# Kernel tuning notes

Measured on AMD Instinct MI355X. Metric: run time of the kernel, lower is better.

## Reference

```python
import jax, jax.numpy as jnp
import numpy as np

N = 50000
E = 600000
D_IN = 128
HID = 128
OUT = 64


def setup_inputs() -> dict:
    key = jax.random.key(0)
    ks = jax.random.split(key, 12)
    x = jax.random.normal(ks[0], (N, D_IN), dtype=jnp.float32)
    edge_index = jax.random.randint(ks[1], (2, E), 0, N, dtype=jnp.int32)
    def lin(k, fan_in, fan_out):
        lim = 1.0 / np.sqrt(fan_in)
        kw, kb = jax.random.split(k)
        W = jax.random.uniform(kw, (fan_in, fan_out), minval=-lim, maxval=lim, dtype=jnp.float32)
        b = jax.random.uniform(kb, (fan_out,), minval=-lim, maxval=lim, dtype=jnp.float32)
        return W, b
    W1, b1 = lin(ks[2], D_IN, HID)
    W2, b2 = lin(ks[3], HID, HID)
    W3, b3 = lin(ks[4], HID, HID)
    fcW, fcb = lin(ks[5], HID, OUT)
    return {"x": x, "edge_index": edge_index, "W1": W1, "b1": b1,
            "W2": W2, "b2": b2, "W3": W3, "b3": b3, "fcW": fcW, "fcb": fcb}


def _gcn_prep(edge_index):
    # add self loops, compute symmetric normalization deg^-1/2 * deg^-1/2
    loop = jnp.arange(N, dtype=edge_index.dtype)
    src = jnp.concatenate([edge_index[0], loop])
    dst = jnp.concatenate([edge_index[1], loop])
    deg = jax.ops.segment_sum(jnp.ones_like(dst, dtype=jnp.float32), dst, num_segments=N)
    dinv = jnp.where(deg > 0, jax.lax.rsqrt(deg), 0.0)
    norm = dinv[src] * dinv[dst]  # [E+N]
    return src, dst, norm


def _gcn_layer(x, src, dst, norm, W, b):
    h = x @ W                      # [N, F_out]
    msg = h[src] * norm[:, None]   # gather + scale, [E+N, F_out]
    agg = jax.ops.segment_sum(msg, dst, num_segments=N)
    return agg + b


def reference(x, edge_index, W1, b1, W2, b2, W3, b3, fcW, fcb):
    src, dst, norm = _gcn_prep(edge_index)
    x = jax.nn.relu(_gcn_layer(x, src, dst, norm, W1, b1))
    x = jax.nn.relu(_gcn_layer(x, src, dst, norm, W2, b2))
    x = jax.nn.relu(_gcn_layer(x, src, dst, norm, W3, b3))
    virtual_node_embedding = x[-1]  # last node's embedding [HID]
    out = virtual_node_embedding @ fcW + fcb  # [OUT]
    return out
```

## Files before the change

kernel.cpp:

```cpp
#include <hip/hip_runtime.h>

#define NF 128
#define OUTF 64

#define M2 1
#define M1 2

#define CAP_F2 2048
#define CAP_E3 4096
#define CAP_F1 32768
#define CAP_E2 65536
#define CAP_E1 262144


__global__ void k_scan1(const int* __restrict__ src, const int* __restrict__ dst,
                        int E, int last, int* __restrict__ mark, int* __restrict__ deg,
                        int* __restrict__ cnt, int* __restrict__ F2,
                        int2* __restrict__ E3l, int2* __restrict__ E2l)
{
    const int gtid = blockIdx.x * blockDim.x + threadIdx.x;
    if (gtid == 0) {
        atomicOr(&mark[last], M2);
        int q = atomicAdd(&cnt[0], 1);
        if (q < CAP_F2) F2[q] = last;
        int r = atomicAdd(&cnt[3], 1);
        if (r < CAP_E2) E2l[r] = make_int2(last, last);
        int e = atomicAdd(&cnt[1], 1);
        if (e < CAP_E3) E3l[e] = make_int2(last, last);
    }

    auto hit = [&](int d, int i) {
        atomicAdd(&deg[d], 1);
        if (d == last) {
            int s = src[i];
            int p = atomicAdd(&cnt[1], 1);
            if (p < CAP_E3) E3l[p] = make_int2(s, d);
            if (s != last && !(atomicOr(&mark[s], M2) & M2)) {
                int q = atomicAdd(&cnt[0], 1);
                if (q < CAP_F2) F2[q] = s;
                int r = atomicAdd(&cnt[3], 1);
                if (r < CAP_E2) E2l[r] = make_int2(s, s);
            }
        }
    };

    const int nq = E >> 2;
    if ((((uintptr_t)dst) & 15) == 0) {
        if (gtid < nq) {
            int4 d4 = ((const int4*)dst)[gtid];
            int i = gtid << 2;
            hit(d4.x, i); hit(d4.y, i + 1); hit(d4.z, i + 2); hit(d4.w, i + 3);
        }
        if (gtid == 0)
            for (int i = nq << 2; i < E; ++i) hit(dst[i], i);
    } else {
        for (int k = 0; k < 4; ++k) {
            int i = gtid * 4 + k;
            if (i < E) hit(dst[i], i);
        }
    }
}

__global__ void k_scan2(const int* __restrict__ src, const int* __restrict__ dst,
                        int E, int* __restrict__ mark, int* __restrict__ cnt,
                        const int* __restrict__ F2, int* __restrict__ F1,
                        int2* __restrict__ E2l, int2* __restrict__ E1l)
{
    const int gtid = blockIdx.x * blockDim.x + threadIdx.x;

    {
        int sc = cnt[0]; if (sc > CAP_F2) sc = CAP_F2;
        if (gtid < sc) {
            int v = F2[gtid];
            if (!(atomicOr(&mark[v], M1) & M1)) {
                int p = atomicAdd(&cnt[2], 1);
                if (p < CAP_F1) F1[p] = v;
                int r = atomicAdd(&cnt[5], 1);
                if (r < CAP_E1) E1l[r] = make_int2(v, v);
            }
        }
    }

    auto hit = [&](int d, int i) {
        if (mark[d] & M2) {
            int s = src[i];
            int p = atomicAdd(&cnt[3], 1);
            if (p < CAP_E2) E2l[p] = make_int2(s, d);
            if (!(atomicOr(&mark[s], M1) & M1)) {
                int q = atomicAdd(&cnt[2], 1);
                if (q < CAP_F1) F1[q] = s;
                int r = atomicAdd(&cnt[5], 1);
                if (r < CAP_E1) E1l[r] = make_int2(s, s);
            }
        }
    };

    const int nq = E >> 2;
    if ((((uintptr_t)dst) & 15) == 0) {
        if (gtid < nq) {
            int4 d4 = ((const int4*)dst)[gtid];
            int i = gtid << 2;
            hit(d4.x, i); hit(d4.y, i + 1); hit(d4.z, i + 2); hit(d4.w, i + 3);
        }
        if (gtid == 0)
            for (int i = nq << 2; i < E; ++i) hit(dst[i], i);
    } else {
        for (int k = 0; k < 4; ++k) {
            int i = gtid * 4 + k;
            if (i < E) hit(dst[i], i);
        }
    }
}

__global__ void k_scan3(const int* __restrict__ src, const int* __restrict__ dst,
                        int E, const int* __restrict__ mark, int* __restrict__ cnt,
                        const int* __restrict__ F1, const int* __restrict__ F2,
                        int2* __restrict__ E1l,
                        float* __restrict__ AGG1, float* __restrict__ AGG2)
{
    const int gtid = blockIdx.x * blockDim.x + threadIdx.x;

    {
        int f1 = cnt[2]; if (f1 > CAP_F1) f1 = CAP_F1;
        if (gtid < f1 * NF)
            AGG1[(size_t)F1[gtid >> 7] * NF + (gtid & 127)] = 0.f;
        int f2 = cnt[0]; if (f2 > CAP_F2) f2 = CAP_F2;
        if (gtid < f2 * NF)
            AGG2[(size_t)F2[gtid >> 7] * NF + (gtid & 127)] = 0.f;
    }

    auto hit = [&](int d, int i) {
        if (mark[d] & M1) {
            int s = src[i];
            int p = atomicAdd(&cnt[5], 1);
            if (p < CAP_E1) E1l[p] = make_int2(s, d);
        }
    };

    const int nq = E >> 2;
    if ((((uintptr_t)dst) & 15) == 0) {
        if (gtid < nq) {
            int4 d4 = ((const int4*)dst)[gtid];
            int i = gtid << 2;
            hit(d4.x, i); hit(d4.y, i + 1); hit(d4.z, i + 2); hit(d4.w, i + 3);
        }
        if (gtid == 0)
            for (int i = nq << 2; i < E; ++i) hit(dst[i], i);
    } else {
        for (int k = 0; k < 4; ++k) {
            int i = gtid * 4 + k;
            if (i < E) hit(dst[i], i);
        }
    }
}

__global__ __launch_bounds__(256) void k_gemv(
    const int2* __restrict__ Elist, const int* __restrict__ cntPtr, int cap,
    const float* __restrict__ Xin, const float* __restrict__ bias,
    const float* __restrict__ W, const int* __restrict__ deg,
    float* __restrict__ AGG)
{
    __shared__ float wsm[128][128];
    int ecnt = *cntPtr; if (ecnt > cap) ecnt = cap;
    if ((int)blockIdx.x * 4 >= ecnt) return;

    const int t = threadIdx.x;
    {
        const float4* W4 = (const float4*)W;
        float4* S4 = (float4*)&wsm[0][0];
        #pragma unroll
        for (int it = 0; it < 16; ++it) S4[it * 256 + t] = W4[it * 256 + t];
    }
    __syncthreads();

    const int wave = t >> 6, lane = t & 63;
    const int wstride = gridDim.x * 4;
    for (int e = blockIdx.x * 4 + wave; e < ecnt; e += wstride) {
        int2 ed = Elist[e];
        float w = rsqrtf(1.f + (float)deg[ed.x]) * rsqrtf(1.f + (float)deg[ed.y]);
        size_t so = (size_t)ed.x * NF;
        float x0 = Xin[so + lane];
        float x1 = Xin[so + lane + 64];
        if (bias) {
            x0 = fmaxf(x0 + bias[lane],      0.f);
            x1 = fmaxf(x1 + bias[lane + 64], 0.f);
        }
        float a0 = 0.f, a1 = 0.f;
        #pragma unroll 16
        for (int k = 0; k < 64; ++k) {
            float xk = __shfl(x0, k);
            a0 += xk * wsm[k][lane];
            a1 += xk * wsm[k][lane + 64];
        }
        #pragma unroll 16
        for (int k = 0; k < 64; ++k) {
            float xk = __shfl(x1, k);
            a0 += xk * wsm[k + 64][lane];
            a1 += xk * wsm[k + 64][lane + 64];
        }
        size_t off = (size_t)ed.y * NF;
        atomicAdd(&AGG[off + lane],      w * a0);
        atomicAdd(&AGG[off + lane + 64], w * a1);
    }
}

__global__ __launch_bounds__(256) void k_tail(
    const int2* __restrict__ E3l, const int* __restrict__ cntPtr, int cap,
    const float* __restrict__ AGG2, const float* __restrict__ b2,
    const float* __restrict__ W3, const float* __restrict__ b3,
    const float* __restrict__ fcW, const float* __restrict__ fcb,
    const int* __restrict__ deg, int last, float* __restrict__ out)
{
    __shared__ float wsm[128][128];
    const int t = threadIdx.x;
    {
        const float4* W4 = (const float4*)W3;
        float4* S4 = (float4*)&wsm[0][0];
        #pragma unroll
        for (int it = 0; it < 16; ++it) S4[it * 256 + t] = W4[it * 256 + t];
    }
    __syncthreads();

    const int wave = t >> 6, lane = t & 63;
    int e3 = *cntPtr; if (e3 > cap) e3 = cap;
    const float dl = rsqrtf(1.f + (float)deg[last]);

    float acc0 = 0.f, acc1 = 0.f;
    for (int e = wave; e < e3; e += 4) {
        int s = E3l[e].x;
        float w = rsqrtf(1.f + (float)deg[s]) * dl;
        size_t so = (size_t)s * NF;
        float x0 = fmaxf(AGG2[so + lane]      + b2[lane],      0.f);
        float x1 = fmaxf(AGG2[so + lane + 64] + b2[lane + 64], 0.f);
        float a0 = 0.f, a1 = 0.f;
        #pragma unroll 16
        for (int k = 0; k < 64; ++k) {
            float xk = __shfl(x0, k);
            a0 += xk * wsm[k][lane];
            a1 += xk * wsm[k][lane + 64];
        }
        #pragma unroll 16
        for (int k = 0; k < 64; ++k) {
            float xk = __shfl(x1, k);
            a0 += xk * wsm[k + 64][lane];
            a1 += xk * wsm[k + 64][lane + 64];
        }
        acc0 += w * a0;
        acc1 += w * a1;
    }
    __syncthreads();
    wsm[wave][lane]      = acc0;
    wsm[wave][lane + 64] = acc1;
    __syncthreads();
    if (t < NF) {
        float s4 = wsm[0][t] + wsm[1][t] + wsm[2][t] + wsm[3][t];
        wsm[8][t] = fmaxf(s4 + b3[t], 0.f);
    }
    __syncthreads();
    if (t < OUTF) {
        float acc = fcb[t];
        #pragma unroll 16
        for (int k = 0; k < NF; ++k) acc += wsm[8][k] * fcW[k * OUTF + t];
        out[t] = acc;
    }
}


extern "C" void kernel_launch(void* const* d_in, const int* in_sizes, int n_in,
                              void* d_out, int out_size, void* d_ws, size_t ws_size,
                              hipStream_t stream)
{
    const float* x    = (const float*)d_in[0];
    const int*   ei   = (const int*)d_in[1];
    const float* W1   = (const float*)d_in[2];
    const float* b1   = (const float*)d_in[3];
    const float* W2   = (const float*)d_in[4];
    const float* b2   = (const float*)d_in[5];
    const float* W3   = (const float*)d_in[6];
    const float* b3   = (const float*)d_in[7];
    const float* fcW  = (const float*)d_in[8];
    const float* fcb  = (const float*)d_in[9];
    float* out = (float*)d_out;

    const int n = in_sizes[0] / NF;
    const int E = in_sizes[1] / 2;
    const int* src = ei;
    const int* dst = ei + E;
    const int last = n - 1;

    char* wp = (char*)d_ws;
    auto alloc = [&](size_t bytes) -> void* {
        void* r = (void*)wp;
        wp += (bytes + 255) & ~(size_t)255;
        return r;
    };
    int*   deg  = (int*)alloc((size_t)n * 4);
    int*   mark = (int*)alloc((size_t)n * 4);
    int*   cnt  = (int*)alloc(64 * 4);
    size_t zbytes = (char*)wp - (char*)deg;

    int*   F2   = (int*) alloc(CAP_F2 * 4);
    int2*  E3   = (int2*)alloc(CAP_E3 * 8);
    int*   F1   = (int*) alloc(CAP_F1 * 4);
    int2*  E2   = (int2*)alloc(CAP_E2 * 8);
    int2*  E1   = (int2*)alloc(CAP_E1 * 8);
    float* AGG1 = (float*)alloc((size_t)n * NF * 4);
    float* AGG2 = (float*)alloc((size_t)n * NF * 4);

    hipMemsetAsync(deg, 0, zbytes, stream);

    const int B = 256;
    const int SB = ((E + 3) / 4 + B - 1) / B;

    k_scan1<<<SB, B, 0, stream>>>(src, dst, E, last, mark, deg, cnt, F2, E3, E2);
    k_scan2<<<SB, B, 0, stream>>>(src, dst, E, mark, cnt, F2, F1, E2, E1);
    k_scan3<<<SB, B, 0, stream>>>(src, dst, E, mark, cnt, F1, F2, E1, AGG1, AGG2);

    k_gemv<<<256, B, 0, stream>>>(E1, &cnt[5], CAP_E1, x, nullptr, W1, deg, AGG1);
    k_gemv<<<64,  B, 0, stream>>>(E2, &cnt[3], CAP_E2, AGG1, b1, W2, deg, AGG2);

    k_tail<<<1, B, 0, stream>>>(E3, &cnt[1], CAP_E3, AGG2, b2, W3, b3,
                                fcW, fcb, deg, last, out);
}
```

Baseline: 166.5 us.

## Fuse layer-1 edge scan into GEMV and merge layer-2 with tail kernel

Drops the third scan kernel and the E1 edge list. The layer-1 GEMV now scans dst directly with wave ballots and processes matching edges inline, and AGG rows are zeroed when nodes are first discovered. Layer 2 and the final tail are merged into a single 1024-thread block, which saves a launch but runs layer 2's roughly 15k edge GEMVs on only one CU. Also risks a race between zeroing a row in scan1 and atomic writes to it.

```diff
diff --git a/kernel.cpp b/kernel.cpp
--- a/kernel.cpp
+++ b/kernel.cpp
@@ -10,19 +10,51 @@
 #define CAP_E3 4096
 #define CAP_F1 32768
 #define CAP_E2 65536
-#define CAP_E1 262144
-
+
+
+__device__ __forceinline__ void zero_row(float* A, int v) {
+    float4* r = (float4*)(A + (size_t)v * NF);
+    #pragma unroll
+    for (int k = 0; k < 32; ++k) r[k] = make_float4(0.f, 0.f, 0.f, 0.f);
+}
+
+__device__ __forceinline__ void gemv_scatter(
+    const float* __restrict__ Xin, int s, float w, int d,
+    float (&wsm)[128][128], int lane, float* __restrict__ AGG)
+{
+    size_t so = (size_t)s * NF;
+    float x0 = Xin[so + lane];
+    float x1 = Xin[so + lane + 64];
+    float a0 = 0.f, a1 = 0.f;
+    #pragma unroll 16
+    for (int k = 0; k < 64; ++k) {
+        float xk = __shfl(x0, k);
+        a0 += xk * wsm[k][lane];
+        a1 += xk * wsm[k][lane + 64];
+    }
+    #pragma unroll 16
+    for (int k = 0; k < 64; ++k) {
+        float xk = __shfl(x1, k);
+        a0 += xk * wsm[k + 64][lane];
+        a1 += xk * wsm[k + 64][lane + 64];
+    }
+    size_t off = (size_t)d * NF;
+    atomicAdd(&AGG[off + lane],      w * a0);
+    atomicAdd(&AGG[off + lane + 64], w * a1);
+}
 
 __global__ void k_scan1(const int* __restrict__ src, const int* __restrict__ dst,
                         int E, int last, int* __restrict__ mark, int* __restrict__ deg,
                         int* __restrict__ cnt, int* __restrict__ F2,
-                        int2* __restrict__ E3l, int2* __restrict__ E2l)
+                        int2* __restrict__ E3l, int2* __restrict__ E2l,
+                        float* __restrict__ AGG2)
 {
     const int gtid = blockIdx.x * blockDim.x + threadIdx.x;
     if (gtid == 0) {
         atomicOr(&mark[last], M2);
         int q = atomicAdd(&cnt[0], 1);
         if (q < CAP_F2) F2[q] = last;
+        zero_row(AGG2, last);
         int r = atomicAdd(&cnt[3], 1);
         if (r < CAP_E2) E2l[r] = make_int2(last, last);
         int e = atomicAdd(&cnt[1], 1);
@@ -38,6 +70,7 @@
             if (s != last && !(atomicOr(&mark[s], M2) & M2)) {
                 int q = atomicAdd(&cnt[0], 1);
                 if (q < CAP_F2) F2[q] = s;
+                zero_row(AGG2, s);
                 int r = atomicAdd(&cnt[3], 1);
                 if (r < CAP_E2) E2l[r] = make_int2(s, s);
             }
@@ -64,7 +97,7 @@
 __global__ void k_scan2(const int* __restrict__ src, const int* __restrict__ dst,
                         int E, int* __restrict__ mark, int* __restrict__ cnt,
                         const int* __restrict__ F2, int* __restrict__ F1,
-                        int2* __restrict__ E2l, int2* __restrict__ E1l)
+                        int2* __restrict__ E2l, float* __restrict__ AGG1)
 {
     const int gtid = blockIdx.x * blockDim.x + threadIdx.x;
 
@@ -75,8 +108,7 @@
             if (!(atomicOr(&mark[v], M1) & M1)) {
                 int p = atomicAdd(&cnt[2], 1);
                 if (p < CAP_F1) F1[p] = v;
-                int r = atomicAdd(&cnt[5], 1);
-                if (r < CAP_E1) E1l[r] = make_int2(v, v);
+                zero_row(AGG1, v);
             }
         }
     }
@@ -89,8 +121,7 @@
             if (!(atomicOr(&mark[s], M1) & M1)) {
                 int q = atomicAdd(&cnt[2], 1);
                 if (q < CAP_F1) F1[q] = s;
-                int r = atomicAdd(&cnt[5], 1);
-                if (r < CAP_E1) E1l[r] = make_int2(s, s);
+                zero_row(AGG1, s);
             }
         }
     };
@@ -112,61 +143,17 @@
     }
 }
 
-__global__ void k_scan3(const int* __restrict__ src, const int* __restrict__ dst,
-                        int E, const int* __restrict__ mark, int* __restrict__ cnt,
-                        const int* __restrict__ F1, const int* __restrict__ F2,
-                        int2* __restrict__ E1l,
-                        float* __restrict__ AGG1, float* __restrict__ AGG2)
-{
-    const int gtid = blockIdx.x * blockDim.x + threadIdx.x;
-
-    {
-        int f1 = cnt[2]; if (f1 > CAP_F1) f1 = CAP_F1;
-        if (gtid < f1 * NF)
-            AGG1[(size_t)F1[gtid >> 7] * NF + (gtid & 127)] = 0.f;
-        int f2 = cnt[0]; if (f2 > CAP_F2) f2 = CAP_F2;
-        if (gtid < f2 * NF)
-            AGG2[(size_t)F2[gtid >> 7] * NF + (gtid & 127)] = 0.f;
-    }
-
-    auto hit = [&](int d, int i) {
-        if (mark[d] & M1) {
-            int s = src[i];
-            int p = atomicAdd(&cnt[5], 1);
-            if (p < CAP_E1) E1l[p] = make_int2(s, d);
-        }
-    };
-
-    const int nq = E >> 2;
-    if ((((uintptr_t)dst) & 15) == 0) {
-        if (gtid < nq) {
-            int4 d4 = ((const int4*)dst)[gtid];
-            int i = gtid << 2;
-            hit(d4.x, i); hit(d4.y, i + 1); hit(d4.z, i + 2); hit(d4.w, i + 3);
-        }
-        if (gtid == 0)
-            for (int i = nq << 2; i < E; ++i) hit(dst[i], i);
-    } else {
-        for (int k = 0; k < 4; ++k) {
-            int i = gtid * 4 + k;
-            if (i < E) hit(dst[i], i);
-        }
-    }
-}
-
-__global__ __launch_bounds__(256) void k_gemv(
-    const int2* __restrict__ Elist, const int* __restrict__ cntPtr, int cap,
-    const float* __restrict__ Xin, const float* __restrict__ bias,
-    const float* __restrict__ W, const int* __restrict__ deg,
-    float* __restrict__ AGG)
+__global__ __launch_bounds__(256) void k_l1(
+    const int* __restrict__ src, const int* __restrict__ dst, int E,
+    const int* __restrict__ mark, const int* __restrict__ deg,
+    const int* __restrict__ cnt, const int* __restrict__ F1,
+    const float* __restrict__ x, const float* __restrict__ W1,
+    float* __restrict__ AGG1)
 {
     __shared__ float wsm[128][128];
-    int ecnt = *cntPtr; if (ecnt > cap) ecnt = cap;
-    if ((int)blockIdx.x * 4 >= ecnt) return;
-
     const int t = threadIdx.x;
     {
-        const float4* W4 = (const float4*)W;
+        const float4* W4 = (const float4*)W1;
         float4* S4 = (float4*)&wsm[0][0];
         #pragma unroll
         for (int it = 0; it < 16; ++it) S4[it * 256 + t] = W4[it * 256 + t];
@@ -174,17 +161,100 @@
     __syncthreads();
 
     const int wave = t >> 6, lane = t & 63;
-    const int wstride = gridDim.x * 4;
-    for (int e = blockIdx.x * 4 + wave; e < ecnt; e += wstride) {
-        int2 ed = Elist[e];
+    const int wg = blockIdx.x * 4 + wave;
+    const int nw = gridDim.x * 4;
+
+    int f1 = cnt[2]; if (f1 > CAP_F1) f1 = CAP_F1;
+    for (int idx = wg; idx < f1; idx += nw) {
+        int v = F1[idx];
+        float w = 1.f / (1.f + (float)deg[v]);
+        gemv_scatter(x, v, w, v, wsm, lane, AGG1);
+    }
+
+    const int nq = E >> 2;
+    const int4* d4p = (const int4*)dst;
+    const bool vec4 = ((((uintptr_t)dst) & 15) == 0);
+    if (vec4) {
+        for (int q0 = wg * 64; q0 < nq; q0 += nw * 64) {
+            int q = q0 + lane;
+            int4 d4 = make_int4(-1, -1, -1, -1);
+            if (q < nq) d4 = d4p[q];
+            #pragma unroll
+            for (int sub = 0; sub < 4; ++sub) {
+                int d = (sub == 0) ? d4.x : (sub == 1) ? d4.y : (sub == 2) ? d4.z : d4.w;
+                bool hit = false; int s = 0;
+                if (q < nq) {
+                    hit = (mark[d] & M1) != 0;
+                    if (hit) s = src[(q << 2) + sub];
+                }
+                unsigned long long m = __ballot(hit);
+                while (m) {
+                    int j = __ffsll(m) - 1; m &= m - 1;
+                    int sb = __shfl(s, j), db = __shfl(d, j);
+                    float w = rsqrtf(1.f + (float)deg[sb]) * rsqrtf(1.f + (float)deg[db]);
+                    gemv_scatter(x, sb, w, db, wsm, lane, AGG1);
+                }
+            }
+        }
+        if (blockIdx.x == 0 && wave == 0) {
+            for (int i = nq << 2; i < E; ++i) {
+                int d = dst[i];
+                if (mark[d] & M1) {
+                    int s = src[i];
+                    float w = rsqrtf(1.f + (float)deg[s]) * rsqrtf(1.f + (float)deg[d]);
+                    gemv_scatter(x, s, w, d, wsm, lane, AGG1);
+                }
+            }
+        }
+    } else {
+        for (int i0 = wg * 64; i0 < E; i0 += nw * 64) {
+            int i = i0 + lane;
+            bool hit = false; int s = 0, d = -1;
+            if (i < E) {
+                d = dst[i];
+                hit = (mark[d] & M1) != 0;
+                if (hit) s = src[i];
+            }
+            unsigned long long m = __ballot(hit);
+            while (m) {
+                int j = __ffsll(m) - 1; m &= m - 1;
+                int sb = __shfl(s, j), db = __shfl(d, j);
+                float w = rsqrtf(1.f + (float)deg[sb]) * rsqrtf(1.f + (float)deg[db]);
+                gemv_scatter(x, sb, w, db, wsm, lane, AGG1);
+            }
+        }
+    }
+}
+
+__global__ __launch_bounds__(1024) void k_l2tail(
+    const int2* __restrict__ E2l, const int2* __restrict__ E3l,
+    const int* __restrict__ cnt,
+    const float* __restrict__ AGG1, const float* __restrict__ b1,
+    const float* __restrict__ W2, const float* __restrict__ b2,
+    const float* __restrict__ W3, const float* __restrict__ b3,
+    const float* __restrict__ fcW, const float* __restrict__ fcb,
+    const int* __restrict__ deg, int last,
+    float* __restrict__ AGG2, float* __restrict__ out)
+{
+    __shared__ float wsm[128][128];
+    const int t = threadIdx.x;
+    const int wave = t >> 6, lane = t & 63;
+
+    {
+        const float4* W4 = (const float4*)W2;
+        float4* S4 = (float4*)&wsm[0][0];
+        #pragma unroll
+        for (int it = 0; it < 4; ++it) S4[it * 1024 + t] = W4[it * 1024 + t];
+    }
+    __syncthreads();
+
+    int e2 = cnt[3]; if (e2 > CAP_E2) e2 = CAP_E2;
+    for (int e = wave; e < e2; e += 16) {
+        int2 ed = E2l[e];
         float w = rsqrtf(1.f + (float)deg[ed.x]) * rsqrtf(1.f + (float)deg[ed.y]);
         size_t so = (size_t)ed.x * NF;
-        float x0 = Xin[so + lane];
-        float x1 = Xin[so + lane + 64];
-        if (bias) {
-            x0 = fmaxf(x0 + bias[lane],      0.f);
-            x1 = fmaxf(x1 + bias[lane + 64], 0.f);
-        }
+        float x0 = fmaxf(AGG1[so + lane]      + b1[lane],      0.f);
+        float x1 = fmaxf(AGG1[so + lane + 64] + b1[lane + 64], 0.f);
         float a0 = 0.f, a1 = 0.f;
         #pragma unroll 16
         for (int k = 0; k < 64; ++k) {
@@ -199,34 +269,24 @@
             a1 += xk * wsm[k + 64][lane + 64];
         }
         size_t off = (size_t)ed.y * NF;
-        atomicAdd(&AGG[off + lane],      w * a0);
-        atomicAdd(&AGG[off + lane + 64], w * a1);
-    }
-}
-
-__global__ __launch_bounds__(256) void k_tail(
-    const int2* __restrict__ E3l, const int* __restrict__ cntPtr, int cap,
-    const float* __restrict__ AGG2, const float* __restrict__ b2,
-    const float* __restrict__ W3, const float* __restrict__ b3,
-    const float* __restrict__ fcW, const float* __restrict__ fcb,
-    const int* __restrict__ deg, int last, float* __restrict__ out)
-{
-    __shared__ float wsm[128][128];
-    const int t = threadIdx.x;
+        atomicAdd(&AGG2[off + lane],      w * a0);
+        atomicAdd(&AGG2[off + lane + 64], w * a1);
+    }
+    __threadfence();
+    __syncthreads();
+
     {
         const float4* W4 = (const float4*)W3;
         float4* S4 = (float4*)&wsm[0][0];
         #pragma unroll
-        for (int it = 0; it < 16; ++it) S4[it * 256 + t] = W4[it * 256 + t];
-    }
-    __syncthreads();
-
-    const int wave = t >> 6, lane = t & 63;
-    int e3 = *cntPtr; if (e3 > cap) e3 = cap;
+        for (int it = 0; it < 4; ++it) S4[it * 1024 + t] = W4[it * 1024 + t];
+    }
+    __syncthreads();
+
+    int e3 = cnt[1]; if (e3 > CAP_E3) e3 = CAP_E3;
     const float dl = rsqrtf(1.f + (float)deg[last]);
-
     float acc0 = 0.f, acc1 = 0.f;
-    for (int e = wave; e < e3; e += 4) {
+    for (int e = wave; e < e3; e += 16) {
         int s = E3l[e].x;
         float w = rsqrtf(1.f + (float)deg[s]) * dl;
         size_t so = (size_t)s * NF;
@@ -253,14 +313,16 @@
     wsm[wave][lane + 64] = acc1;
     __syncthreads();
     if (t < NF) {
-        float s4 = wsm[0][t] + wsm[1][t] + wsm[2][t] + wsm[3][t];
-        wsm[8][t] = fmaxf(s4 + b3[t], 0.f);
+        float s = 0.f;
+        #pragma unroll
+        for (int k = 0; k < 16; ++k) s += wsm[k][t];
+        wsm[16][t] = fmaxf(s + b3[t], 0.f);
     }
     __syncthreads();
     if (t < OUTF) {
         float acc = fcb[t];
         #pragma unroll 16
-        for (int k = 0; k < NF; ++k) acc += wsm[8][k] * fcW[k * OUTF + t];
+        for (int k = 0; k < NF; ++k) acc += wsm[16][k] * fcW[k * OUTF + t];
         out[t] = acc;
     }
 }
@@ -303,7 +365,6 @@
     int2*  E3   = (int2*)alloc(CAP_E3 * 8);
     int*   F1   = (int*) alloc(CAP_F1 * 4);
     int2*  E2   = (int2*)alloc(CAP_E2 * 8);
-    int2*  E1   = (int2*)alloc(CAP_E1 * 8);
     float* AGG1 = (float*)alloc((size_t)n * NF * 4);
     float* AGG2 = (float*)alloc((size_t)n * NF * 4);
 
@@ -312,13 +373,9 @@
     const int B = 256;
     const int SB = ((E + 3) / 4 + B - 1) / B;
 
-    k_scan1<<<SB, B, 0, stream>>>(src, dst, E, last, mark, deg, cnt, F2, E3, E2);
-    k_scan2<<<SB, B, 0, stream>>>(src, dst, E, mark, cnt, F2, F1, E2, E1);
-    k_scan3<<<SB, B, 0, stream>>>(src, dst, E, mark, cnt, F1, F2, E1, AGG1, AGG2);
-
-    k_gemv<<<256, B, 0, stream>>>(E1, &cnt[5], CAP_E1, x, nullptr, W1, deg, AGG1);
-    k_gemv<<<64,  B, 0, stream>>>(E2, &cnt[3], CAP_E2, AGG1, b1, W2, deg, AGG2);
-
-    k_tail<<<1, B, 0, stream>>>(E3, &cnt[1], CAP_E3, AGG2, b2, W3, b3,
-                                fcW, fcb, deg, last, out);
-}
+    k_scan1<<<SB, B, 0, stream>>>(src, dst, E, last, mark, deg, cnt, F2, E3, E2, AGG2);
+    k_scan2<<<SB, B, 0, stream>>>(src, dst, E, mark, cnt, F2, F1, E2, AGG1);
+    k_l1   <<<256, B, 0, stream>>>(src, dst, E, mark, deg, cnt, F1, x, W1, AGG1);
+    k_l2tail<<<1, 1024, 0, stream>>>(E2, E3, cnt, AGG1, b1, W2, b2, W3, b3,
+                                     fcW, fcb, deg, last, AGG2, out);
+}
```

Result: slower. 232.2 us (+39.5%).
